# Kernel optimization log

Measured on AMD Instinct MI355X. Metric: run time of the kernel, lower is better.

The kernel has to match this reference:

```python
import jax, jax.numpy as jnp
import numpy as np

EPS = 1e-5
LAMB = 1.0
N_VARS = 40000
N_EDGES = 200000
N_CONF = 100000
FEAT = 128
DOM = 4
T_MAX = 3


def setup_inputs() -> dict:
    key = jax.random.key(0)
    ks = jax.random.split(key, 16)
    # initial node states: torch.rand then row-normalized (F.normalize dim=1)
    s = jax.random.uniform(ks[0], (N_VARS, FEAT), dtype=jnp.float32)
    state0 = s / jnp.maximum(jnp.linalg.norm(s, axis=1, keepdims=True), 1e-12)
    def lin(k, fan_in, shape):
        return jax.random.normal(k, shape, dtype=jnp.float32) / np.sqrt(fan_in)
    inp = {
        'state0': state0,
        'W1': lin(ks[1], 2 * FEAT, (2 * FEAT, FEAT)),
        'b1': jnp.zeros((FEAT,), jnp.float32),
        'W2': lin(ks[2], FEAT, (FEAT, FEAT)),
        'b2': jnp.zeros((FEAT,), jnp.float32),
        'ln_g': jnp.ones((FEAT,), jnp.float32),
        'ln_b': jnp.zeros((FEAT,), jnp.float32),
        'bn_g': jnp.ones((FEAT,), jnp.float32),
        'bn_b': jnp.zeros((FEAT,), jnp.float32),
        'Wd': lin(ks[3], FEAT, (FEAT, DOM)),
        'bd': jnp.zeros((DOM,), jnp.float32),
        # positive relation/confidence matrices so -log(...) is finite
        'relation': jax.random.uniform(ks[4], (DOM, DOM), jnp.float32, 0.1, 1.0),
        'confidence_mat': jax.random.uniform(ks[5], (DOM, DOM), jnp.float32, 0.1, 1.0),
        # positive degrees (divisor)
        'degrees': jax.random.uniform(ks[6], (N_VARS,), jnp.float32, 1.0, 33.0),
        'idx_left': jax.random.randint(ks[7], (N_EDGES,), 0, N_VARS, jnp.int32),
        'idx_right': jax.random.randint(ks[8], (N_EDGES,), 0, N_VARS, jnp.int32),
        'idx_left_pos': jax.random.randint(ks[9], (N_CONF,), 0, N_VARS, jnp.int32),
        'idx_right_pos': jax.random.randint(ks[10], (N_CONF,), 0, N_VARS, jnp.int32),
        'iterations': T_MAX,
    }
    return inp


def reference(state0, W1, b1, W2, b2, ln_g, ln_b, bn_g, bn_b, Wd, bd,
              relation, confidence_mat, degrees,
              idx_left, idx_right, idx_left_pos, idx_right_pos, iterations):
    N, F = state0.shape
    E = idx_left.shape[0]
    degs = degrees[:, None]

    def mlp(x):  # Linear-ReLU-Linear-ReLU-LayerNorm
        h = jax.nn.relu(x @ W1 + b1)
        h = jax.nn.relu(h @ W2 + b2)
        mu = jnp.mean(h, axis=-1, keepdims=True)
        var = jnp.var(h, axis=-1, keepdims=True)  # biased, like torch LayerNorm
        return ln_g * (h - mu) * jax.lax.rsqrt(var + EPS) + ln_b

    state = state0
    logits_list = []
    for _ in range(iterations):
        xl = state[idx_left]          # [E, F] gather
        xr = state[idx_right]
        # mpnn(in_right=xl, in_left=xr): in_lr = cat(xr, xl); in_rl = cat(xl, xr)
        msg = jnp.concatenate([jnp.concatenate([xr, xl], axis=1),
                               jnp.concatenate([xl, xr], axis=1)], axis=0)  # [2E, 2F]
        h = mlp(msg)
        agg = (jnp.zeros((N, F), state.dtype)
               .at[idx_left].add(h[:E])
               .at[idx_right].add(h[E:]))  # scatter-add messages
        rec = agg / degs
        # BatchNorm1d, training mode (batch stats over nodes)
        mu = jnp.mean(rec, axis=0)
        var = jnp.var(rec, axis=0)
        state = bn_g * (rec - mu) * jax.lax.rsqrt(var + EPS) + bn_b
        logits_list.append(state @ Wd + bd)

    phi = jax.nn.softmax(jnp.stack(logits_list, axis=1), axis=2)  # [N, T, D]
    T, D = phi.shape[1], phi.shape[2]
    all_phi = phi.reshape(N, T * D)

    def pair_loss(mat, il, ir, denom):
        pl = all_phi[il].reshape(-1, D)   # [E*T, D]
        pr = all_phi[ir].reshape(-1, D)
        s = jnp.sum((pl @ mat) * pr, axis=1)
        return jnp.sum(-jnp.log(s)) / denom

    n_conflicts = jnp.float32(E)
    n_confidence = jnp.float32(idx_left_pos.shape[0])
    loss = (pair_loss(relation, idx_left, idx_right, n_conflicts)
            + LAMB * pair_loss(confidence_mat, idx_left_pos, idx_right_pos, 10.0 * n_confidence))

    assignment = jnp.argmax(phi, axis=2).astype(jnp.int32)  # [N, T]
    valid = relation[assignment[idx_left], assignment[idx_right]]  # [E, T]
    edge_conflicts = 1.0 - valid
    n_conf = jnp.sum(edge_conflicts[:, -1])
    conflict_ratio = n_conf / n_conflicts
    return (loss, conflict_ratio, phi, edge_conflicts, assignment[:, -1], n_conf)
```

## Files before the change

kernel.cpp:

```cpp
#include <hip/hip_runtime.h>
#include <math.h>

#define N_VARS 40000
#define FEAT 128
#define N_EDGES 200000
#define N_MSG (2*N_EDGES)
#define N_CONFP 100000
#define T_ITERS 3
#define EPSF 1e-5f

#define NB_CONF 782
#define NB_PAIR 1172
#define NB_STAT 157
#define NB_STAT2 625
#define NB_MSGB 3125
#define OUT_TOTAL 1120003
#define NCONF_SLOT 1120002

typedef short short8 __attribute__((ext_vector_type(8)));
typedef float floatx4 __attribute__((ext_vector_type(4)));
typedef unsigned short ushort4v __attribute__((ext_vector_type(4)));

__device__ __forceinline__ float scrub0(float x){
  unsigned u = __float_as_uint(x);
  return ((u & 0x7F800000u) == 0x7F800000u) ? 0.f : x;
}
__device__ __forceinline__ unsigned short f2bf_rne(float x){
  unsigned u = __float_as_uint(x);
  u += 0x7FFFu + ((u >> 16) & 1u);
  return (unsigned short)(u >> 16);
}
__device__ __forceinline__ float bf2f(unsigned short h){
  return __uint_as_float(((unsigned)h) << 16);
}
__device__ __forceinline__ unsigned cvtpk(float lo, float hi){
  unsigned r;
  asm("v_cvt_pk_bf16_f32 %0, %1, %2" : "=v"(r) : "v"(lo), "v"(hi));
  return r;
}

__global__ __launch_bounds__(256) void k_zero_int(int* __restrict__ p, int n){
  int i = blockIdx.x*256 + threadIdx.x;
  if (i < n) p[i] = 0;
}

__global__ __launch_bounds__(256) void k_hist(const int* __restrict__ idxL,
    const int* __restrict__ idxR, int* __restrict__ cnt){
  int m = blockIdx.x*256 + threadIdx.x;
  if (m < N_MSG){
    int t = (m < N_EDGES) ? idxL[m] : idxR[m - N_EDGES];
    atomicAdd(&cnt[t], 1);
  }
}
__global__ __launch_bounds__(256) void k_scan1(const int* __restrict__ cnt,
    int* __restrict__ pos, int* __restrict__ blk_tot){
  const int tid = threadIdx.x;
  const int idx = blockIdx.x*256 + tid;
  int v = (idx < N_VARS) ? cnt[idx] : 0;
  __shared__ int sh[256];
  sh[tid] = v;
  __syncthreads();
#pragma unroll
  for (int o = 1; o < 256; o <<= 1){
    int add = (tid >= o) ? sh[tid - o] : 0;
    __syncthreads();
    sh[tid] += add;
    __syncthreads();
  }
  if (idx < N_VARS) pos[idx] = sh[tid] - v;
  if (tid == 255) blk_tot[blockIdx.x] = sh[255];
}
__global__ __launch_bounds__(256) void k_scan2(const int* __restrict__ blk_tot,
    int* __restrict__ blk_off){
  const int tid = threadIdx.x;
  int v = (tid < NB_STAT) ? blk_tot[tid] : 0;
  __shared__ int sh[256];
  sh[tid] = v;
  __syncthreads();
#pragma unroll
  for (int o = 1; o < 256; o <<= 1){
    int add = (tid >= o) ? sh[tid - o] : 0;
    __syncthreads();
    sh[tid] += add;
    __syncthreads();
  }
  if (tid < NB_STAT) blk_off[tid] = sh[tid] - v;
}
__global__ __launch_bounds__(256) void k_scan3(int* __restrict__ pos,
    const int* __restrict__ blk_off){
  const int idx = blockIdx.x*256 + threadIdx.x;
  if (idx < N_VARS) pos[idx] += blk_off[blockIdx.x];
}
__global__ __launch_bounds__(256) void k_fill(const int* __restrict__ idxL,
    const int* __restrict__ idxR, int* __restrict__ pos,
    int2* __restrict__ pairs){
  int m = blockIdx.x*256 + threadIdx.x;
  if (m < N_MSG){
    int e = (m < N_EDGES) ? m : (m - N_EDGES);
    int l = idxL[e], r = idxR[e];
    int t = (m < N_EDGES) ? l : r;
    int o = (m < N_EDGES) ? r : l;
    int slot = atomicAdd(&pos[t], 1);
    pairs[slot] = make_int2(t, o);
  }
}

__global__ __launch_bounds__(256) void k_prep2(const float* __restrict__ W2,
                                               const float* __restrict__ W1,
                                               unsigned short* __restrict__ W2pack,
                                               unsigned short* __restrict__ W1pack){
  if (blockIdx.x < 8){
    int gid = blockIdx.x*256 + threadIdx.x;
    int lane = gid & 63;
    int ks = (gid >> 6) & 3;
    int ntg = gid >> 8;
    int kbase = ks*32 + (lane >> 4)*8;
    int n = ntg*16 + (lane & 15);
#pragma unroll
    for (int j = 0; j < 8; ++j)
      W2pack[gid*8 + j] = f2bf_rne(W2[(kbase + j)*FEAT + n]);
  } else {
    int gid = (blockIdx.x - 8)*256 + threadIdx.x;
    int lane = gid & 63;
    int ks = (gid >> 6) & 3;
    int ntg = gid >> 8;
    int kbase = ks*32 + (lane >> 4)*8;
    int n = ntg*16 + (lane & 15);
#pragma unroll
    for (int j = 0; j < 8; ++j){
      int k = kbase + j;
      float v = (n < 128) ? W1[k*FEAT + n] : W1[(128 + k)*FEAT + (n - 128)];
      W1pack[gid*8 + j] = f2bf_rne(v);
    }
  }
}

#define X_STRIDE 136
__global__ __launch_bounds__(256) void k_pq(const float* __restrict__ xf,
                                            const unsigned short* __restrict__ xb,
                                            int src_f32,
                                            const unsigned short* __restrict__ W1pack,
                                            const float* __restrict__ b1v,
                                            unsigned short* __restrict__ PQb,
                                            float* __restrict__ red,
                                            float4* __restrict__ recz){
  __shared__ __align__(16) unsigned short Xbf[32*X_STRIDE];
  const int tid = threadIdx.x;
  const int row0 = blockIdx.x * 32;
  if (blockIdx.x == 0) red[tid] = 0.f;
  {
    const int zid = blockIdx.x*256 + tid;
#pragma unroll
    for (int i = 0; i < 4; ++i)
      recz[zid + i*320000] = make_float4(0.f,0.f,0.f,0.f);
  }
  if (src_f32){
    const int c4 = (tid & 31)*4, g8 = tid >> 5;
#pragma unroll
    for (int r = 0; r < 4; ++r){
      int row = g8*4 + r;
      const float4 v = *(const float4*)&xf[(row0 + row)*FEAT + c4];
      uint2 uu;
      uu.x = cvtpk(v.x, v.y);
      uu.y = cvtpk(v.z, v.w);
      *(uint2*)&Xbf[row*X_STRIDE + c4] = uu;
    }
  } else {
    const int c8 = (tid & 15)*8, g16 = tid >> 4;
#pragma unroll
    for (int r = 0; r < 2; ++r){
      int row = r*16 + g16;
      *(short8*)&Xbf[row*X_STRIDE + c8] = *(const short8*)&xb[(row0 + row)*FEAT + c8];
    }
  }
  __syncthreads();
  const int w = tid >> 6, lane = tid & 63;
  const int quad = lane >> 4, mcol = lane & 15;
  float bi0 = 0.f, bi1 = 0.f, bi2 = 0.f, bi3 = 0.f;
  if (w >= 2){
    int nb = (w - 2)*64 + mcol;
    bi0 = b1v[nb]; bi1 = b1v[nb + 16]; bi2 = b1v[nb + 32]; bi3 = b1v[nb + 48];
  }
#pragma unroll
  for (int mt = 0; mt < 2; ++mt){
    floatx4 a0 = {bi0,bi0,bi0,bi0};
    floatx4 a1 = {bi1,bi1,bi1,bi1};
    floatx4 a2 = {bi2,bi2,bi2,bi2};
    floatx4 a3 = {bi3,bi3,bi3,bi3};
#pragma unroll
    for (int ks = 0; ks < 4; ++ks){
      short8 a = *(const short8*)&Xbf[(mt*16 + mcol)*X_STRIDE + ks*32 + quad*8];
      const unsigned short* bp = W1pack + ((w*16 + ks)*64 + lane)*8;
      short8 b0 = *(const short8*)(bp);
      short8 b1 = *(const short8*)(bp + 2048);
      short8 b2 = *(const short8*)(bp + 4096);
      short8 b3 = *(const short8*)(bp + 6144);
      a0 = __builtin_amdgcn_mfma_f32_16x16x32_bf16(a, b0, a0, 0, 0, 0);
      a1 = __builtin_amdgcn_mfma_f32_16x16x32_bf16(a, b1, a1, 0, 0, 0);
      a2 = __builtin_amdgcn_mfma_f32_16x16x32_bf16(a, b2, a2, 0, 0, 0);
      a3 = __builtin_amdgcn_mfma_f32_16x16x32_bf16(a, b3, a3, 0, 0, 0);
    }
#pragma unroll
    for (int reg = 0; reg < 4; ++reg){
      unsigned u01 = cvtpk(a0[reg], a1[reg]);
      unsigned u23 = cvtpk(a2[reg], a3[reg]);
      size_t base = (size_t)(row0 + mt*16 + quad*4 + reg)*(2*FEAT) + w*64 + mcol;
      PQb[base]      = (unsigned short)u01;
      PQb[base + 16] = (unsigned short)(u01 >> 16);
      PQb[base + 32] = (unsigned short)u23;
      PQb[base + 48] = (unsigned short)(u23 >> 16);
    }
  }
}

#define U_STRIDE 136
#define ZT_STRIDE 68

__device__ __forceinline__ void conv_store_U(const short8* pb, const short8* qb,
                                             unsigned short* Ubf, int c8, int g16){
#pragma unroll
  for (int r = 0; r < 4; ++r){
    int row = r*16 + g16;
    float f[8];
#pragma unroll
    for (int j = 0; j < 8; ++j)
      f[j] = fmaxf(bf2f((unsigned short)pb[r][j]) + bf2f((unsigned short)qb[r][j]), 0.f);
    uint4 uu;
    uu.x = cvtpk(f[0], f[1]);
    uu.y = cvtpk(f[2], f[3]);
    uu.z = cvtpk(f[4], f[5]);
    uu.w = cvtpk(f[6], f[7]);
    *(uint4*)&Ubf[row*U_STRIDE + c8] = uu;
  }
}

__device__ __forceinline__ void mfma_ln_zt(const unsigned short* Ubf,
    unsigned short* Zbf, const unsigned short* __restrict__ W2pack,
    const float* __restrict__ b2v, const float* __restrict__ ln_g,
    const float* __restrict__ ln_b, int tid){
  const int w = tid >> 6, lane = tid & 63;
  const int quad = lane >> 4, mcol = lane & 15;
  const int rbase = w*16;
  floatx4 acc[8];
#pragma unroll
  for (int nt = 0; nt < 8; ++nt){
    float b = b2v[nt*16 + mcol];
    acc[nt] = (floatx4){b, b, b, b};
  }
#pragma unroll
  for (int ks = 0; ks < 4; ++ks){
    short8 a = *(const short8*)&Ubf[(rbase + mcol)*U_STRIDE + ks*32 + quad*8];
#pragma unroll
    for (int nt = 0; nt < 8; ++nt){
      short8 b = *(const short8*)(W2pack + ((nt*4 + ks)*64 + lane)*8);
      acc[nt] = __builtin_amdgcn_mfma_f32_16x16x32_bf16(a, b, acc[nt], 0, 0, 0);
    }
  }
  float z[8][4];
#pragma unroll
  for (int nt = 0; nt < 8; ++nt){
#pragma unroll
    for (int reg = 0; reg < 4; ++reg) z[nt][reg] = fmaxf(acc[nt][reg], 0.f);
  }
  float ps[4], pq[4];
#pragma unroll
  for (int reg = 0; reg < 4; ++reg){
    ps[reg] = 0.f; pq[reg] = 0.f;
#pragma unroll
    for (int nt = 0; nt < 8; ++nt){
      ps[reg] += z[nt][reg];
      pq[reg] += z[nt][reg]*z[nt][reg];
    }
  }
#pragma unroll
  for (int o = 1; o < 16; o <<= 1){
#pragma unroll
    for (int reg = 0; reg < 4; ++reg){
      ps[reg] += __shfl_xor(ps[reg], o);
      pq[reg] += __shfl_xor(pq[reg], o);
    }
  }
  float muv[4], rvv[4];
#pragma unroll
  for (int reg = 0; reg < 4; ++reg){
    float mu = ps[reg] * (1.f/FEAT);
    float var = fmaxf(pq[reg] * (1.f/FEAT) - mu*mu, 0.f);
    muv[reg] = mu;
    rvv[reg] = rsqrtf(var + EPSF);
  }
#pragma unroll
  for (int nt = 0; nt < 8; ++nt){
    float lg = ln_g[nt*16 + mcol];
    float lb = ln_b[nt*16 + mcol];
    float o0 = scrub0(lg*(z[nt][0] - muv[0])*rvv[0] + lb);
    float o1 = scrub0(lg*(z[nt][1] - muv[1])*rvv[1] + lb);
    float o2 = scrub0(lg*(z[nt][2] - muv[2])*rvv[2] + lb);
    float o3 = scrub0(lg*(z[nt][3] - muv[3])*rvv[3] + lb);
    uint2 u; u.x = cvtpk(o0, o1); u.y = cvtpk(o2, o3);
    *(uint2*)&Zbf[(nt*16 + mcol)*ZT_STRIDE + rbase + quad*4] = u;
  }
}

__device__ __forceinline__ void phaseC(const unsigned short* Zbf,
    const int* sTa_t, const float* sDinv_t, const unsigned* brk2,
    int eprev, int enext, float* __restrict__ rec, int tid){
  const int col = tid & 127, h = tid >> 7;
  const int rbeg = h*32;
  const unsigned bm = __builtin_amdgcn_readfirstlane(brk2[h]);
  ushort4v rv4[8];
#pragma unroll
  for (int k = 0; k < 8; ++k)
    rv4[k] = *(const ushort4v*)&Zbf[col*ZT_STRIDE + rbeg + k*4];
  float accv = 0.f;
  int cur = sTa_t[rbeg];
  bool part = (rbeg == 0) ? (eprev == cur) : (sTa_t[rbeg-1] == cur);
#pragma unroll
  for (int i = 0; i < 32; ++i){
    accv += bf2f((unsigned short)rv4[i >> 2][i & 3]);
    const bool realbrk = (bm >> i) & 1u;
    if ((i == 31) | realbrk){
      const int r = rbeg + i;
      bool cont = (i == 31) && ((r == 63) ? (enext == cur) : !realbrk);
      float v = accv * sDinv_t[r];
      float* dst = &rec[(size_t)cur*FEAT + col];
      if (part | cont) atomicAdd(dst, v);
      else *dst = v;
      accv = 0.f;
      part = false;
      if (i < 31) cur = sTa_t[r + 1];
    }
  }
}

__global__ __launch_bounds__(256, 4) void k_msgagg(const unsigned short* __restrict__ PQb,
    const unsigned short* __restrict__ W2pack,
    const float* __restrict__ b2v, const float* __restrict__ ln_g, const float* __restrict__ ln_b,
    const int2* __restrict__ pairs, const float* __restrict__ degrees,
    float* __restrict__ rec){
  __shared__ __align__(16) unsigned short Ubf[64*U_STRIDE];
  __shared__ __align__(16) unsigned short Zbf[128*ZT_STRIDE];
  __shared__ int sTa[2][64];
  __shared__ float sDinv[2][64];
  __shared__ int sE[2][2];
  __shared__ unsigned sBrk[2][2];
  const int tid = threadIdx.x;
  const int s0 = blockIdx.x * 128;
  const int c8 = (tid & 15)*8, g16 = tid >> 4;
  int2 prA[4], prB[4];
#pragma unroll
  for (int r = 0; r < 4; ++r){
    prA[r] = pairs[s0 + r*16 + g16];
    prB[r] = pairs[s0 + 64 + r*16 + g16];
  }
  short8 pbA[4], qbA[4];
#pragma unroll
  for (int r = 0; r < 4; ++r){
    pbA[r] = *(const short8*)&PQb[(size_t)prA[r].y*(2*FEAT) + c8];
    qbA[r] = *(const short8*)&PQb[(size_t)prA[r].x*(2*FEAT) + FEAT + c8];
  }
  const int w = tid >> 6, lane = tid & 63;
  if (w == 1 || w == 2){
    const int tl = w - 1;
    int ta = pairs[s0 + tl*64 + lane].x;
    sTa[tl][lane] = ta;
    sDinv[tl][lane] = 1.f / degrees[ta];
    int tn = __shfl_down(ta, 1);
    bool d = (lane == 63) ? true : (tn != ta);
    unsigned long long b = __ballot(d);
    if (lane == 0){ sBrk[tl][0] = (unsigned)b; sBrk[tl][1] = (unsigned)(b >> 32); }
  } else if (w == 3 && lane < 4){
    int tl = lane >> 1, sd = lane & 1;
    int idx = s0 + tl*64 + (sd ? 64 : -1);
    sE[tl][sd] = (idx < 0 || idx >= N_MSG) ? -1 : pairs[idx].x;
  }
  conv_store_U(pbA, qbA, Ubf, c8, g16);
  short8 pbB[4], qbB[4];
#pragma unroll
  for (int r = 0; r < 4; ++r){
    pbB[r] = *(const short8*)&PQb[(size_t)prB[r].y*(2*FEAT) + c8];
    qbB[r] = *(const short8*)&PQb[(size_t)prB[r].x*(2*FEAT) + FEAT + c8];
  }
  __syncthreads();
  mfma_ln_zt(Ubf, Zbf, W2pack, b2v, ln_g, ln_b, tid);
  __syncthreads();
  phaseC(Zbf, sTa[0], sDinv[0], sBrk[0], sE[0][0], sE[0][1], rec, tid);
  conv_store_U(pbB, qbB, Ubf, c8, g16);
  __syncthreads();
  mfma_ln_zt(Ubf, Zbf, W2pack, b2v, ln_g, ln_b, tid);
  __syncthreads();
  phaseC(Zbf, sTa[1], sDinv[1], sBrk[1], sE[1][0], sE[1][1], rec, tid);
}

__global__ __launch_bounds__(256) void k_edge(const unsigned short* __restrict__ PQb,
    const unsigned short* __restrict__ W2pack,
    const float* __restrict__ b2v, const float* __restrict__ ln_g, const float* __restrict__ ln_b,
    const int* __restrict__ idxL, const int* __restrict__ idxR,
    float* __restrict__ agg){
  __shared__ __align__(16) unsigned short Ubf[32*U_STRIDE];
  __shared__ float sS[64], sQ[64];
  __shared__ int sTa[32], sTb[32];
  const int tid = threadIdx.x;
  const int m0 = blockIdx.x * 32;
  if (tid < 32){
    int m = m0 + tid;
    int e = (m < N_EDGES) ? m : (m - N_EDGES);
    int l = idxL[e], r = idxR[e];
    sTa[tid] = (m < N_EDGES) ? l : r;
    sTb[tid] = (m < N_EDGES) ? r : l;
  }
  __syncthreads();
  {
    const int c8 = (tid & 15)*8, g16 = tid >> 4;
#pragma unroll
    for (int r = 0; r < 2; ++r){
      int row = r*16 + g16;
      short8 pb = *(const short8*)&PQb[sTb[row]*(2*FEAT) + c8];
      short8 qb = *(const short8*)&PQb[sTa[row]*(2*FEAT) + FEAT + c8];
      float f[8];
#pragma unroll
      for (int j = 0; j < 8; ++j)
        f[j] = fmaxf(bf2f((unsigned short)pb[j]) + bf2f((unsigned short)qb[j]), 0.f);
      uint4 uu;
      uu.x = cvtpk(f[0], f[1]);
      uu.y = cvtpk(f[2], f[3]);
      uu.z = cvtpk(f[4], f[5]);
      uu.w = cvtpk(f[6], f[7]);
      *(uint4*)&Ubf[row*U_STRIDE + c8] = uu;
    }
  }
  __syncthreads();
  const int w = tid >> 6, lane = tid & 63;
  const int mt = w & 1, nhalf = w >> 1;
  const int quad = lane >> 4, mcol = lane & 15;
  float bb0 = b2v[nhalf*64 + 0*16 + mcol];
  float bb1 = b2v[nhalf*64 + 1*16 + mcol];
  float bb2 = b2v[nhalf*64 + 2*16 + mcol];
  float bb3 = b2v[nhalf*64 + 3*16 + mcol];
  floatx4 acc0 = {bb0,bb0,bb0,bb0};
  floatx4 acc1 = {bb1,bb1,bb1,bb1};
  floatx4 acc2 = {bb2,bb2,bb2,bb2};
  floatx4 acc3 = {bb3,bb3,bb3,bb3};
#pragma unroll
  for (int ks = 0; ks < 4; ++ks){
    short8 a = *(const short8*)&Ubf[(mt*16 + mcol)*U_STRIDE + ks*32 + quad*8];
    const unsigned short* bp = W2pack + ((nhalf*4*256) + ks*64 + lane)*8;
    short8 bq0 = *(const short8*)(bp);
    short8 bq1 = *(const short8*)(bp + 2048);
    short8 bq2 = *(const short8*)(bp + 4096);
    short8 bq3 = *(const short8*)(bp + 6144);
    acc0 = __builtin_amdgcn_mfma_f32_16x16x32_bf16(a, bq0, acc0, 0, 0, 0);
    acc1 = __builtin_amdgcn_mfma_f32_16x16x32_bf16(a, bq1, acc1, 0, 0, 0);
    acc2 = __builtin_amdgcn_mfma_f32_16x16x32_bf16(a, bq2, acc2, 0, 0, 0);
    acc3 = __builtin_amdgcn_mfma_f32_16x16x32_bf16(a, bq3, acc3, 0, 0, 0);
  }
  float z[4][4];
#pragma unroll
  for (int nt = 0; nt < 4; ++nt){
    floatx4 a4 = (nt == 0) ? acc0 : (nt == 1) ? acc1 : (nt == 2) ? acc2 : acc3;
#pragma unroll
    for (int reg = 0; reg < 4; ++reg) z[nt][reg] = fmaxf(a4[reg], 0.f);
  }
  float ps[4], pq[4];
#pragma unroll
  for (int reg = 0; reg < 4; ++reg){
    ps[reg] = z[0][reg] + z[1][reg] + z[2][reg] + z[3][reg];
    pq[reg] = z[0][reg]*z[0][reg] + z[1][reg]*z[1][reg] + z[2][reg]*z[2][reg] + z[3][reg]*z[3][reg];
  }
#pragma unroll
  for (int o = 1; o < 16; o <<= 1){
#pragma unroll
    for (int reg = 0; reg < 4; ++reg){
      ps[reg] += __shfl_xor(ps[reg], o);
      pq[reg] += __shfl_xor(pq[reg], o);
    }
  }
  if (mcol == 0){
#pragma unroll
    for (int reg = 0; reg < 4; ++reg){
      int row = mt*16 + quad*4 + reg;
      sS[nhalf*32 + row] = ps[reg];
      sQ[nhalf*32 + row] = pq[reg];
    }
  }
  __syncthreads();
  int colv[4]; float lgv[4], lbv[4];
#pragma unroll
  for (int nt = 0; nt < 4; ++nt){
    colv[nt] = nhalf*64 + nt*16 + mcol;
    lgv[nt] = ln_g[colv[nt]];
    lbv[nt] = ln_b[colv[nt]];
  }
#pragma unroll
  for (int reg = 0; reg < 4; ++reg){
    int row = mt*16 + quad*4 + reg;
    float s = sS[row] + sS[32 + row];
    float q = sQ[row] + sQ[32 + row];
    float mu = s * (1.f/FEAT);
    float var = fmaxf(q * (1.f/FEAT) - mu*mu, 0.f);
    float rv = rsqrtf(var + EPSF);
    int a = sTa[row];
#pragma unroll
    for (int nt = 0; nt < 4; ++nt){
      float o = scrub0(lgv[nt]*(z[nt][reg] - mu)*rv + lbv[nt]);
      atomicAdd(&agg[a*FEAT + colv[nt]], o);
    }
  }
}

__global__ __launch_bounds__(256) void k_stats(const float* __restrict__ src,
    const float* __restrict__ degrees, int divide, float* __restrict__ red){
  const int tid = threadIdx.x;
  const int j = tid & 127, half_sel = tid >> 7;
  const int n0 = blockIdx.x * 64;
  float s1 = 0.f, s2 = 0.f;
  for (int i = half_sel; i < 64; i += 2){
    int n = n0 + i;
    float v = src[n*FEAT + j];
    if (divide) v /= degrees[n];
    s1 += v;
    s2 += v*v;
  }
  __shared__ float sh1[256], sh2[256];
  sh1[tid] = s1; sh2[tid] = s2;
  __syncthreads();
  if (half_sel == 0){
    atomicAdd(&red[j],       sh1[tid] + sh1[tid+128]);
    atomicAdd(&red[128 + j], sh2[tid] + sh2[tid+128]);
  }
}

__global__ __launch_bounds__(256) void k_bn(const float* __restrict__ src,
    const float* __restrict__ degrees, int divide, const float* __restrict__ red,
    const float* __restrict__ bn_g, const float* __restrict__ bn_b,
    const float* __restrict__ Wd, const float* __restrict__ bd,
    unsigned short* __restrict__ state_bf, int* __restrict__ asg,
    float* __restrict__ out_phi, float* __restrict__ out_asg, int t){
  const int w = threadIdx.x >> 6, l = threadIdx.x & 63;
  const int n = blockIdx.x*4 + w;
  const float invN = 1.f / (float)N_VARS;
  float mu0 = red[l]*invN,     mu1 = red[l+64]*invN;
  float v0  = fmaxf(red[128+l]*invN    - mu0*mu0, 0.f);
  float v1  = fmaxf(red[128+l+64]*invN - mu1*mu1, 0.f);
  float rv0 = rsqrtf(v0 + EPSF);
  float rv1 = rsqrtf(v1 + EPSF);
  float dinv = divide ? (1.f / degrees[n]) : 1.f;
  float r0 = src[n*FEAT + l]    * dinv;
  float r1 = src[n*FEAT + l+64] * dinv;
  float s0 = scrub0(bn_g[l]   *(r0 - mu0)*rv0 + bn_b[l]);
  float s1 = scrub0(bn_g[l+64]*(r1 - mu1)*rv1 + bn_b[l+64]);
  state_bf[n*FEAT + l]    = f2bf_rne(s0);
  state_bf[n*FEAT + l+64] = f2bf_rne(s1);
  float p[4];
#pragma unroll
  for (int d = 0; d < 4; ++d)
    p[d] = s0*Wd[l*4 + d] + s1*Wd[(l+64)*4 + d];
#pragma unroll
  for (int o = 32; o > 0; o >>= 1){
#pragma unroll
    for (int d = 0; d < 4; ++d) p[d] += __shfl_xor(p[d], o);
  }
  if (l == 0){
    float lg[4];
#pragma unroll
    for (int d = 0; d < 4; ++d) lg[d] = scrub0(p[d] + bd[d]);
    float mx = fmaxf(fmaxf(lg[0],lg[1]), fmaxf(lg[2],lg[3]));
    float ex[4]; float ssum = 0.f;
#pragma unroll
    for (int d = 0; d < 4; ++d){ ex[d] = expf(lg[d] - mx); ssum += ex[d]; }
    float inv = 1.f / ssum;
    int am = 0; float bv = -1.f;
#pragma unroll
    for (int d = 0; d < 4; ++d){
      float pv = scrub0(ex[d]*inv);
      out_phi[n*12 + t*4 + d] = pv;
      if (pv > bv){ bv = pv; am = d; }
    }
    asg[n*3 + t] = am;
    if (t == 2) out_asg[n] = (float)am;
  }
}

__global__ __launch_bounds__(256) void k_lossconf(const float* __restrict__ phi,
    const int* __restrict__ iL, const int* __restrict__ iR,
    const int* __restrict__ iLp, const int* __restrict__ iRp,
    const float* __restrict__ rel, const float* __restrict__ conf,
    const int* __restrict__ asg, float* __restrict__ out_ec,
    float* __restrict__ part_l1, float* __restrict__ part_l2,
    float* __restrict__ part_conf){
  if (blockIdx.x < NB_PAIR){
    const int e = blockIdx.x*256 + threadIdx.x;
    float p1 = 0.f, p2 = 0.f;
    if (e < N_EDGES + N_CONFP){
      const int isrel = (e < N_EDGES);
      const int l = isrel ? iL[e] : iLp[e - N_EDGES];
      const int r = isrel ? iR[e] : iRp[e - N_EDGES];
      const float* M = isrel ? rel : conf;
      const float2* plp = (const float2*)(phi + (size_t)l*12);
      const float2* prp = (const float2*)(phi + (size_t)r*12);
      float L[12], R[12];
#pragma unroll
      for (int k = 0; k < 6; ++k){
        float2 a = plp[k], b = prp[k];
        L[2*k] = a.x; L[2*k+1] = a.y;
        R[2*k] = b.x; R[2*k+1] = b.y;
      }
      float acc = 0.f;
#pragma unroll
      for (int tt = 0; tt < 3; ++tt){
        const float* a = L + tt*4;
        const float* b = R + tt*4;
        float s = 0.f;
#pragma unroll
        for (int j = 0; j < 4; ++j){
          float tj = a[0]*M[0*4+j] + a[1]*M[1*4+j] + a[2]*M[2*4+j] + a[3]*M[3*4+j];
          s += tj*b[j];
        }
        s = scrub0(s); s = fmaxf(s, 1e-35f);
        acc -= __logf(s);
      }
      if (isrel) p1 = acc; else p2 = acc;
    }
    __shared__ float sh1[256], sh2[256];
    sh1[threadIdx.x] = p1; sh2[threadIdx.x] = p2;
    __syncthreads();
    for (int k = 128; k > 0; k >>= 1){
      if (threadIdx.x < k){
        sh1[threadIdx.x] += sh1[threadIdx.x + k];
        sh2[threadIdx.x] += sh2[threadIdx.x + k];
      }
      __syncthreads();
    }
    if (threadIdx.x == 0){
      part_l1[blockIdx.x] = sh1[0];
      part_l2[blockIdx.x] = sh2[0];
    }
  } else {
    const int bid = blockIdx.x - NB_PAIR;
    const int e = bid*256 + threadIdx.x;
    float c2 = 0.f;
    if (e < N_EDGES){
      int l = iL[e], r = iR[e];
#pragma unroll
      for (int tt = 0; tt < 3; ++tt){
        int ai = asg[l*3+tt] & 3, bi = asg[r*3+tt] & 3;
        float c = scrub0(1.f - rel[ai*4 + bi]);
        out_ec[e*3 + tt] = c;
        if (tt == 2) c2 = c;
      }
    }
    __shared__ float sh[256];
    sh[threadIdx.x] = c2;
    __syncthreads();
    for (int k = 128; k > 0; k >>= 1){
      if (threadIdx.x < k) sh[threadIdx.x] += sh[threadIdx.x + k];
      __syncthreads();
    }
    if (threadIdx.x == 0) part_conf[bid] = sh[0];
  }
}

__global__ __launch_bounds__(256) void k_fin(const float* __restrict__ part_conf,
    const float* __restrict__ part_l1, const float* __restrict__ part_l2,
    float* __restrict__ out){
  const int tid = threadIdx.x;
  float a = 0.f, ca = 0.f, b = 0.f, cb = 0.f, c = 0.f;
  for (int i = tid; i < NB_PAIR; i += 256){
    float y = part_l1[i] - ca; float t = a + y; ca = (t - a) - y; a = t;
    float y2 = part_l2[i] - cb; float t2 = b + y2; cb = (t2 - b) - y2; b = t2;
  }
  for (int i = tid; i < NB_CONF; i += 256) c += part_conf[i];
  __shared__ float sh1[256], sh2[256], sh3[256];
  sh1[tid] = a; sh2[tid] = b; sh3[tid] = c;
  __syncthreads();
  for (int k = 128; k > 0; k >>= 1){
    if (tid < k){
      sh1[tid] += sh1[tid + k];
      sh2[tid] += sh2[tid + k];
      sh3[tid] += sh3[tid + k];
    }
    __syncthreads();
  }
  if (tid == 0){
    out[0] = sh1[0]/(float)N_EDGES + sh2[0]/(10.f*(float)N_CONFP);
    float nc = sh3[0];
    out[NCONF_SLOT] = nc;
    out[1] = nc / (float)N_EDGES;
  }
}

extern "C" void kernel_launch(void* const* d_in, const int* in_sizes, int n_in,
                              void* d_out, int out_size, void* d_ws, size_t ws_size,
                              hipStream_t stream){
  const float* state0  = (const float*)d_in[0];
  const float* W1      = (const float*)d_in[1];
  const float* b1v     = (const float*)d_in[2];
  const float* W2      = (const float*)d_in[3];
  const float* b2v     = (const float*)d_in[4];
  const float* ln_g    = (const float*)d_in[5];
  const float* ln_b    = (const float*)d_in[6];
  const float* bn_g    = (const float*)d_in[7];
  const float* bn_b    = (const float*)d_in[8];
  const float* Wd      = (const float*)d_in[9];
  const float* bd      = (const float*)d_in[10];
  const float* rel     = (const float*)d_in[11];
  const float* confm   = (const float*)d_in[12];
  const float* degrees = (const float*)d_in[13];
  const int* idxL = (const int*)d_in[14];
  const int* idxR = (const int*)d_in[15];
  const int* iLp  = (const int*)d_in[16];
  const int* iRp  = (const int*)d_in[17];

  char* ws = (char*)d_ws;
  unsigned short* state_bf = (unsigned short*)(ws);
  unsigned short* PQb  = (unsigned short*)(ws + 10240000);
  float*  recagg    = (float*)(ws + 30720000);
  int*    asg       = (int*)  (ws + 51200000);
  float*  red       = (float*)(ws + 51840768);
  float*  part_l1   = (float*)(ws + 51841792);
  float*  part_l2   = (float*)(ws + 51855860);
  float*  part_conf = (float*)(ws + 51869928);
  unsigned short* W2pack = (unsigned short*)(ws + 51873056);
  unsigned short* W1pack = (unsigned short*)(ws + 51905824);
  int*    pos       = (int*)(ws + 51971360);
  int*    cnt       = (int*)(ws + 52131360);
  int2*   pairs     = (int2*)(ws + 52291360);
  int*    blk_tot   = (int*)(ws + 55491360);
  int*    blk_off   = (int*)(ws + 55492384);
  const int use_csr = (ws_size >= (size_t)55493408) ? 1 : 0;

  float* out     = (float*)d_out;
  float* out_phi = out + 2;
  float* out_ec  = out + 480002;
  float* out_asg = out + 1080002;

  k_prep2<<<24, 256, 0, stream>>>(W2, W1, W2pack, W1pack);

  if (use_csr){
    k_zero_int<<<NB_STAT, 256, 0, stream>>>(cnt, N_VARS);
    k_hist<<<(N_MSG + 255)/256, 256, 0, stream>>>(idxL, idxR, cnt);
    k_scan1<<<NB_STAT, 256, 0, stream>>>(cnt, pos, blk_tot);
    k_scan2<<<1, 256, 0, stream>>>(blk_tot, blk_off);
    k_scan3<<<NB_STAT, 256, 0, stream>>>(pos, blk_off);
    k_fill<<<(N_MSG + 255)/256, 256, 0, stream>>>(idxL, idxR, pos, pairs);
  }

  for (int t = 0; t < T_ITERS; ++t){
    k_pq<<<N_VARS/32, 256, 0, stream>>>(state0, state_bf, (t == 0) ? 1 : 0, W1pack, b1v,
                                        PQb, red, (float4*)recagg);
    if (use_csr){
      k_msgagg<<<NB_MSGB, 256, 0, stream>>>(PQb, W2pack, b2v, ln_g, ln_b,
                                            pairs, degrees, recagg);
      k_stats<<<NB_STAT2, 256, 0, stream>>>(recagg, degrees, 0, red);
      k_bn<<<N_VARS/4, 256, 0, stream>>>(recagg, degrees, 0, red, bn_g, bn_b, Wd, bd,
                                         state_bf, asg, out_phi, out_asg, t);
    } else {
      k_edge<<<N_MSG/32, 256, 0, stream>>>(PQb, W2pack, b2v, ln_g, ln_b, idxL, idxR, recagg);
      k_stats<<<NB_STAT2, 256, 0, stream>>>(recagg, degrees, 1, red);
      k_bn<<<N_VARS/4, 256, 0, stream>>>(recagg, degrees, 1, red, bn_g, bn_b, Wd, bd,
                                         state_bf, asg, out_phi, out_asg, t);
    }
  }
  k_lossconf<<<NB_PAIR + NB_CONF, 256, 0, stream>>>(out_phi, idxL, idxR, iLp, iRp, rel, confm,
                                                    asg, out_ec, part_l1, part_l2, part_conf);
  k_fin<<<1, 256, 0, stream>>>(part_conf, part_l1, part_l2, out);
}
```

Baseline: 552.3 us.

## Load gathered message rows straight into MFMA A fragments, one 64-row tile per block

Measured after the change: 536.8 us. 1.03x faster.

```diff
diff --git a/kernel.cpp b/kernel.cpp
--- a/kernel.cpp
+++ b/kernel.cpp
@@ -13,13 +13,14 @@
 #define NB_PAIR 1172
 #define NB_STAT 157
 #define NB_STAT2 625
-#define NB_MSGB 3125
+#define NB_MSG64 6250
 #define OUT_TOTAL 1120003
 #define NCONF_SLOT 1120002
 
 typedef short short8 __attribute__((ext_vector_type(8)));
 typedef float floatx4 __attribute__((ext_vector_type(4)));
 typedef unsigned short ushort4v __attribute__((ext_vector_type(4)));
+typedef unsigned uint4v __attribute__((ext_vector_type(4)));
 
 __device__ __forceinline__ float scrub0(float x){
   unsigned u = __float_as_uint(x);
@@ -216,31 +217,57 @@
 #define U_STRIDE 136
 #define ZT_STRIDE 68
 
-__device__ __forceinline__ void conv_store_U(const short8* pb, const short8* qb,
-                                             unsigned short* Ubf, int c8, int g16){
-#pragma unroll
-  for (int r = 0; r < 4; ++r){
-    int row = r*16 + g16;
-    float f[8];
-#pragma unroll
-    for (int j = 0; j < 8; ++j)
-      f[j] = fmaxf(bf2f((unsigned short)pb[r][j]) + bf2f((unsigned short)qb[r][j]), 0.f);
-    uint4 uu;
-    uu.x = cvtpk(f[0], f[1]);
-    uu.y = cvtpk(f[2], f[3]);
-    uu.z = cvtpk(f[4], f[5]);
-    uu.w = cvtpk(f[6], f[7]);
-    *(uint4*)&Ubf[row*U_STRIDE + c8] = uu;
-  }
-}
-
-__device__ __forceinline__ void mfma_ln_zt(const unsigned short* Ubf,
-    unsigned short* Zbf, const unsigned short* __restrict__ W2pack,
-    const float* __restrict__ b2v, const float* __restrict__ ln_g,
-    const float* __restrict__ ln_b, int tid){
+__global__ __launch_bounds__(256) void k_msgagg(const unsigned short* __restrict__ PQb,
+    const unsigned short* __restrict__ W2pack,
+    const float* __restrict__ b2v, const float* __restrict__ ln_g, const float* __restrict__ ln_b,
+    const int2* __restrict__ pairs, const float* __restrict__ degrees,
+    float* __restrict__ rec){
+  __shared__ __align__(16) unsigned short Zbf[128*ZT_STRIDE];
+  __shared__ int sTa[64];
+  __shared__ float sDinv[64];
+  __shared__ int sE[2];
+  __shared__ unsigned sBrk[2];
+  const int tid = threadIdx.x;
+  const int s0 = blockIdx.x * 64;
   const int w = tid >> 6, lane = tid & 63;
   const int quad = lane >> 4, mcol = lane & 15;
   const int rbase = w*16;
+  const int2 pr = pairs[s0 + rbase + mcol];
+  const unsigned short* Prow = PQb + (size_t)pr.y*(2*FEAT) + quad*8;
+  const unsigned short* Qrow = PQb + (size_t)pr.x*(2*FEAT) + FEAT + quad*8;
+  short8 pch[4], qch[4];
+#pragma unroll
+  for (int ks = 0; ks < 4; ++ks){
+    pch[ks] = *(const short8*)(Prow + ks*32);
+    qch[ks] = *(const short8*)(Qrow + ks*32);
+  }
+  if (w == 0){
+    int ta = pairs[s0 + lane].x;
+    sTa[lane] = ta;
+    sDinv[lane] = 1.f / degrees[ta];
+    int tn = __shfl_down(ta, 1);
+    bool d = (lane == 63) ? true : (tn != ta);
+    unsigned long long b = __ballot(d);
+    if (lane == 0){ sBrk[0] = (unsigned)b; sBrk[1] = (unsigned)(b >> 32); }
+    if (lane == 62) sE[0] = (s0 == 0) ? -1 : pairs[s0 - 1].x;
+    if (lane == 63) sE[1] = (s0 + 64 >= N_MSG) ? -1 : pairs[s0 + 64].x;
+  }
+  short8 afr[4];
+#pragma unroll
+  for (int ks = 0; ks < 4; ++ks){
+    uint4v pu = *(const uint4v*)&pch[ks];
+    uint4v qu = *(const uint4v*)&qch[ks];
+    uint4v ou;
+#pragma unroll
+    for (int d = 0; d < 4; ++d){
+      float plo = __uint_as_float(pu[d] << 16);
+      float phi = __uint_as_float(pu[d] & 0xFFFF0000u);
+      float qlo = __uint_as_float(qu[d] << 16);
+      float qhi = __uint_as_float(qu[d] & 0xFFFF0000u);
+      ou[d] = cvtpk(fmaxf(plo + qlo, 0.f), fmaxf(phi + qhi, 0.f));
+    }
+    afr[ks] = *(const short8*)&ou;
+  }
   floatx4 acc[8];
 #pragma unroll
   for (int nt = 0; nt < 8; ++nt){
@@ -249,11 +276,10 @@
   }
 #pragma unroll
   for (int ks = 0; ks < 4; ++ks){
-    short8 a = *(const short8*)&Ubf[(rbase + mcol)*U_STRIDE + ks*32 + quad*8];
 #pragma unroll
     for (int nt = 0; nt < 8; ++nt){
       short8 b = *(const short8*)(W2pack + ((nt*4 + ks)*64 + lane)*8);
-      acc[nt] = __builtin_amdgcn_mfma_f32_16x16x32_bf16(a, b, acc[nt], 0, 0, 0);
+      acc[nt] = __builtin_amdgcn_mfma_f32_16x16x32_bf16(afr[ks], b, acc[nt], 0, 0, 0);
     }
   }
   float z[8][4];
@@ -299,96 +325,35 @@
     uint2 u; u.x = cvtpk(o0, o1); u.y = cvtpk(o2, o3);
     *(uint2*)&Zbf[(nt*16 + mcol)*ZT_STRIDE + rbase + quad*4] = u;
   }
-}
-
-__device__ __forceinline__ void phaseC(const unsigned short* Zbf,
-    const int* sTa_t, const float* sDinv_t, const unsigned* brk2,
-    int eprev, int enext, float* __restrict__ rec, int tid){
-  const int col = tid & 127, h = tid >> 7;
-  const int rbeg = h*32;
-  const unsigned bm = __builtin_amdgcn_readfirstlane(brk2[h]);
-  ushort4v rv4[8];
-#pragma unroll
-  for (int k = 0; k < 8; ++k)
-    rv4[k] = *(const ushort4v*)&Zbf[col*ZT_STRIDE + rbeg + k*4];
-  float accv = 0.f;
-  int cur = sTa_t[rbeg];
-  bool part = (rbeg == 0) ? (eprev == cur) : (sTa_t[rbeg-1] == cur);
-#pragma unroll
-  for (int i = 0; i < 32; ++i){
-    accv += bf2f((unsigned short)rv4[i >> 2][i & 3]);
-    const bool realbrk = (bm >> i) & 1u;
-    if ((i == 31) | realbrk){
-      const int r = rbeg + i;
-      bool cont = (i == 31) && ((r == 63) ? (enext == cur) : !realbrk);
-      float v = accv * sDinv_t[r];
-      float* dst = &rec[(size_t)cur*FEAT + col];
-      if (part | cont) atomicAdd(dst, v);
-      else *dst = v;
-      accv = 0.f;
-      part = false;
-      if (i < 31) cur = sTa_t[r + 1];
-    }
-  }
-}
-
-__global__ __launch_bounds__(256, 4) void k_msgagg(const unsigned short* __restrict__ PQb,
-    const unsigned short* __restrict__ W2pack,
-    const float* __restrict__ b2v, const float* __restrict__ ln_g, const float* __restrict__ ln_b,
-    const int2* __restrict__ pairs, const float* __restrict__ degrees,
-    float* __restrict__ rec){
-  __shared__ __align__(16) unsigned short Ubf[64*U_STRIDE];
-  __shared__ __align__(16) unsigned short Zbf[128*ZT_STRIDE];
-  __shared__ int sTa[2][64];
-  __shared__ float sDinv[2][64];
-  __shared__ int sE[2][2];
-  __shared__ unsigned sBrk[2][2];
-  const int tid = threadIdx.x;
-  const int s0 = blockIdx.x * 128;
-  const int c8 = (tid & 15)*8, g16 = tid >> 4;
-  int2 prA[4], prB[4];
-#pragma unroll
-  for (int r = 0; r < 4; ++r){
-    prA[r] = pairs[s0 + r*16 + g16];
-    prB[r] = pairs[s0 + 64 + r*16 + g16];
-  }
-  short8 pbA[4], qbA[4];
-#pragma unroll
-  for (int r = 0; r < 4; ++r){
-    pbA[r] = *(const short8*)&PQb[(size_t)prA[r].y*(2*FEAT) + c8];
-    qbA[r] = *(const short8*)&PQb[(size_t)prA[r].x*(2*FEAT) + FEAT + c8];
-  }
-  const int w = tid >> 6, lane = tid & 63;
-  if (w == 1 || w == 2){
-    const int tl = w - 1;
-    int ta = pairs[s0 + tl*64 + lane].x;
-    sTa[tl][lane] = ta;
-    sDinv[tl][lane] = 1.f / degrees[ta];
-    int tn = __shfl_down(ta, 1);
-    bool d = (lane == 63) ? true : (tn != ta);
-    unsigned long long b = __ballot(d);
-    if (lane == 0){ sBrk[tl][0] = (unsigned)b; sBrk[tl][1] = (unsigned)(b >> 32); }
-  } else if (w == 3 && lane < 4){
-    int tl = lane >> 1, sd = lane & 1;
-    int idx = s0 + tl*64 + (sd ? 64 : -1);
-    sE[tl][sd] = (idx < 0 || idx >= N_MSG) ? -1 : pairs[idx].x;
-  }
-  conv_store_U(pbA, qbA, Ubf, c8, g16);
-  short8 pbB[4], qbB[4];
-#pragma unroll
-  for (int r = 0; r < 4; ++r){
-    pbB[r] = *(const short8*)&PQb[(size_t)prB[r].y*(2*FEAT) + c8];
-    qbB[r] = *(const short8*)&PQb[(size_t)prB[r].x*(2*FEAT) + FEAT + c8];
-  }
-  __syncthreads();
-  mfma_ln_zt(Ubf, Zbf, W2pack, b2v, ln_g, ln_b, tid);
-  __syncthreads();
-  phaseC(Zbf, sTa[0], sDinv[0], sBrk[0], sE[0][0], sE[0][1], rec, tid);
-  conv_store_U(pbB, qbB, Ubf, c8, g16);
-  __syncthreads();
-  mfma_ln_zt(Ubf, Zbf, W2pack, b2v, ln_g, ln_b, tid);
-  __syncthreads();
-  phaseC(Zbf, sTa[1], sDinv[1], sBrk[1], sE[1][0], sE[1][1], rec, tid);
+  __syncthreads();
+  {
+    const int col = tid & 127, h = tid >> 7;
+    const int rbeg = h*32;
+    const unsigned bm = __builtin_amdgcn_readfirstlane(sBrk[h]);
+    ushort4v rv4[8];
+#pragma unroll
+    for (int k = 0; k < 8; ++k)
+      rv4[k] = *(const ushort4v*)&Zbf[col*ZT_STRIDE + rbeg + k*4];
+    float accv = 0.f;
+    int cur = sTa[rbeg];
+    bool part = (rbeg == 0) ? (sE[0] == cur) : (sTa[rbeg-1] == cur);
+#pragma unroll
+    for (int i = 0; i < 32; ++i){
+      accv += bf2f((unsigned short)rv4[i >> 2][i & 3]);
+      const bool realbrk = (bm >> i) & 1u;
+      if ((i == 31) | realbrk){
+        const int r = rbeg + i;
+        bool cont = (i == 31) && ((r == 63) ? (sE[1] == cur) : !realbrk);
+        float v = accv * sDinv[r];
+        float* dst = &rec[(size_t)cur*FEAT + col];
+        if (part | cont) atomicAdd(dst, v);
+        else *dst = v;
+        accv = 0.f;
+        part = false;
+        if (i < 31) cur = sTa[r + 1];
+      }
+    }
+  }
 }
 
 __global__ __launch_bounds__(256) void k_edge(const unsigned short* __restrict__ PQb,
@@ -748,8 +713,8 @@
     k_pq<<<N_VARS/32, 256, 0, stream>>>(state0, state_bf, (t == 0) ? 1 : 0, W1pack, b1v,
                                         PQb, red, (float4*)recagg);
     if (use_csr){
-      k_msgagg<<<NB_MSGB, 256, 0, stream>>>(PQb, W2pack, b2v, ln_g, ln_b,
-                                            pairs, degrees, recagg);
+      k_msgagg<<<NB_MSG64, 256, 0, stream>>>(PQb, W2pack, b2v, ln_g, ln_b,
+                                             pairs, degrees, recagg);
       k_stats<<<NB_STAT2, 256, 0, stream>>>(recagg, degrees, 0, red);
       k_bn<<<N_VARS/4, 256, 0, stream>>>(recagg, degrees, 0, red, bn_g, bn_b, Wd, bd,
                                          state_bf, asg, out_phi, out_asg, t);
```
